# Performance work log

Measured on AMD Instinct MI355X. Metric: run time of the kernel, lower is better.

Reference implementation:

```python
import jax, jax.numpy as jnp
import numpy as np


def setup_inputs() -> dict:
    key = jax.random.key(0)
    ks = jax.random.split(key, 7)
    B, HW, C, H = 32, 3136, 512, 128
    return {
        "c_embed": jax.random.normal(ks[0], (B * HW, C), dtype=jnp.float32),
        "w_embed": jax.random.normal(ks[1], (B * HW, C), dtype=jnp.float32),
        "h_embed": jax.random.normal(ks[2], (B * HW, C), dtype=jnp.float32),
        "fc1_w": jax.random.normal(ks[3], (H, C), dtype=jnp.float32) * 0.05,
        "fc1_b": jax.random.normal(ks[4], (H,), dtype=jnp.float32) * 0.05,
        "fc2_w": jax.random.normal(ks[5], (3 * C, H), dtype=jnp.float32) * 0.05,
        "fc2_b": jax.random.normal(ks[6], (3 * C,), dtype=jnp.float32) * 0.05,
        "B": 32,
    }


def reference(c_embed, w_embed, h_embed, fc1_w, fc1_b, fc2_w, fc2_b, B):
    N, C = c_embed.shape
    HW = N // B
    # (1) global mean over HW of the sum of the three embeddings -> (B, C)
    s = (c_embed + w_embed + h_embed).reshape(B, HW, C).mean(axis=1)
    # (2) 2-layer MLP: fc1 -> GELU(tanh approx, matching gelu_fast) -> fc2
    y1 = jax.nn.gelu(s @ fc1_w.T + fc1_b, approximate=True)          # (B, hidden)
    logits = y1 @ fc2_w.T + fc2_b                                    # (B, 3*C)
    # (3) 3-way softmax: kernel indexes logits[j*C + c] => layout (B, 3, C),
    #     softmax over the 3 branches
    w = jax.nn.softmax(logits.reshape(B, 3, C), axis=1)              # (B, 3, C)
    w0 = jnp.repeat(w[:, 0, :], HW, axis=0)                          # (B*HW, C)
    w1 = jnp.repeat(w[:, 1, :], HW, axis=0)
    w2 = jnp.repeat(w[:, 2, :], HW, axis=0)
    # (4) broadcast weighted sum
    return c_embed * w0 + w_embed * w1 + h_embed * w2
```

## Files before the change

### kernel.cpp

```cpp
#include <hip/hip_runtime.h>

#define B_      32
#define HW_     3136
#define C_      512
#define H_      128
#define NCHUNK  32
#define ROWS_PER_CHUNK (HW_ / NCHUNK)

__global__ __launch_bounds__(256) void ps_kernel(
    const float* __restrict__ c_e,
    const float* __restrict__ w_e,
    const float* __restrict__ h_e,
    float* __restrict__ partial)
{
    const int blk = blockIdx.x;
    const int b   = blk / NCHUNK;
    const int k   = blk - b * NCHUNK;
    const int t   = threadIdx.x;

    const long row0 = (long)b * HW_ + (long)k * ROWS_PER_CHUNK;
    const float2* __restrict__ c2 = (const float2*)c_e;
    const float2* __restrict__ w2 = (const float2*)w_e;
    const float2* __restrict__ h2 = (const float2*)h_e;

    long base = row0 * (C_ / 2) + t;
    float ax = 0.f, ay = 0.f;
    #pragma unroll 2
    for (int r = 0; r < ROWS_PER_CHUNK; ++r) {
        float2 a = c2[base];
        float2 v = w2[base];
        float2 u = h2[base];
        ax += a.x + v.x + u.x;
        ay += a.y + v.y + u.y;
        base += (C_ / 2);
    }
    float2 o; o.x = ax; o.y = ay;
    ((float2*)partial)[(long)blk * (C_ / 2) + t] = o;
}

__global__ __launch_bounds__(256) void mlp_kernel(
    const float* __restrict__ partial,
    const float* __restrict__ fc1_w,
    const float* __restrict__ fc1_b,
    const float* __restrict__ fc2_w,
    const float* __restrict__ fc2_b,
    float* __restrict__ wbuf)
{
    __shared__ float s_lds[C_];
    __shared__ float y_lds[H_];

    const int b = blockIdx.x;
    const int t = threadIdx.x;

    for (int c = t; c < C_; c += 256) {
        float acc = 0.f;
        #pragma unroll
        for (int k = 0; k < NCHUNK; ++k)
            acc += partial[(long)(b * NCHUNK + k) * C_ + c];
        s_lds[c] = acc * (1.0f / (float)HW_);
    }
    __syncthreads();

    if (t < H_) {
        float acc = fc1_b[t];
        const float* __restrict__ wr = fc1_w + (long)t * C_;
        #pragma unroll 8
        for (int c = 0; c < C_; ++c) acc += s_lds[c] * wr[c];
        const float x  = acc;
        const float u  = 0.7978845608028654f * (x + 0.044715f * x * x * x);
        y_lds[t] = 0.5f * x * (1.0f + tanhf(u));
    }
    __syncthreads();

    for (int c = t; c < C_; c += 256) {
        float lg[3];
        #pragma unroll
        for (int j = 0; j < 3; ++j) {
            const int row = j * C_ + c;
            float acc = fc2_b[row];
            const float* __restrict__ wr = fc2_w + (long)row * H_;
            #pragma unroll 8
            for (int h = 0; h < H_; ++h) acc += y_lds[h] * wr[h];
            lg[j] = acc;
        }
        const float m  = fmaxf(lg[0], fmaxf(lg[1], lg[2]));
        const float e0 = __expf(lg[0] - m);
        const float e1 = __expf(lg[1] - m);
        const float e2 = __expf(lg[2] - m);
        const float inv = 1.0f / (e0 + e1 + e2);
        float* __restrict__ wb = wbuf + (long)b * 3 * C_;
        wb[0 * C_ + c] = e0 * inv;
        wb[1 * C_ + c] = e1 * inv;
        wb[2 * C_ + c] = e2 * inv;
    }
}

__global__ __launch_bounds__(256) void out_kernel(
    const float* __restrict__ c_e,
    const float* __restrict__ w_e,
    const float* __restrict__ h_e,
    const float* __restrict__ wbuf,
    float* __restrict__ out)
{
    const float4* __restrict__ c4 = (const float4*)c_e;
    const float4* __restrict__ w4 = (const float4*)w_e;
    const float4* __restrict__ h4 = (const float4*)h_e;
    float4* __restrict__ o4       = (float4*)out;
    const float4* __restrict__ wb4 = (const float4*)wbuf;

    const int total = B_ * HW_ * (C_ / 4);
    const int stride = gridDim.x * blockDim.x;
    for (int idx = blockIdx.x * blockDim.x + threadIdx.x; idx < total; idx += stride) {
        const int row  = idx >> 7;
        const int col4 = idx & 127;
        const int b    = row / HW_;
        const float4* __restrict__ wb = wb4 + (long)b * (3 * C_ / 4);
        const float4 w0 = wb[col4];
        const float4 w1 = wb[128 + col4];
        const float4 w2 = wb[256 + col4];
        const float4 a = c4[idx];
        const float4 v = w4[idx];
        const float4 u = h4[idx];
        float4 o;
        o.x = a.x * w0.x + v.x * w1.x + u.x * w2.x;
        o.y = a.y * w0.y + v.y * w1.y + u.y * w2.y;
        o.z = a.z * w0.z + v.z * w1.z + u.z * w2.z;
        o.w = a.w * w0.w + v.w * w1.w + u.w * w2.w;
        o4[idx] = o;
    }
}

extern "C" void kernel_launch(void* const* d_in, const int* in_sizes, int n_in,
                              void* d_out, int out_size, void* d_ws, size_t ws_size,
                              hipStream_t stream)
{
    const float* c_e   = (const float*)d_in[0];
    const float* w_e   = (const float*)d_in[1];
    const float* h_e   = (const float*)d_in[2];
    const float* fc1_w = (const float*)d_in[3];
    const float* fc1_b = (const float*)d_in[4];
    const float* fc2_w = (const float*)d_in[5];
    const float* fc2_b = (const float*)d_in[6];
    float* out = (float*)d_out;

    float* partial = (float*)d_ws;
    float* wbuf    = partial + (long)B_ * NCHUNK * C_;

    ps_kernel<<<B_ * NCHUNK, 256, 0, stream>>>(c_e, w_e, h_e, partial);
    mlp_kernel<<<B_, 256, 0, stream>>>(partial, fc1_w, fc1_b, fc2_w, fc2_b, wbuf);
    out_kernel<<<2048, 256, 0, stream>>>(c_e, w_e, h_e, wbuf, out);
}
```

Measured before the change: 328.8 us.

## Widen reduction grid, vectorize to float4, and tile output kernel per batch

The partial-sum kernel now uses float4 loads. Each block splits its rows between two half-blocks and combines them in shared memory, and the chunk count rises from 32 to 98 (falling back if workspace is small) to put more blocks in flight. The output kernel becomes a 2D grid of per-batch tiles that load the softmax weights once per thread, replacing the grid-stride loop that did an integer division per element. The MLP kernel now reads a variable chunk count, so it loses the fully unrolled partial reduction and does more partial reads.

```diff
diff --git a/kernel.cpp b/kernel.cpp
--- a/kernel.cpp
+++ b/kernel.cpp
@@ -1,41 +1,46 @@
 #include <hip/hip_runtime.h>
 
-#define B_      32
-#define HW_     3136
-#define C_      512
-#define H_      128
-#define NCHUNK  32
-#define ROWS_PER_CHUNK (HW_ / NCHUNK)
+#define B_   32
+#define HW_  3136
+#define C_   512
+#define H_   128
 
 __global__ __launch_bounds__(256) void ps_kernel(
-    const float* __restrict__ c_e,
-    const float* __restrict__ w_e,
-    const float* __restrict__ h_e,
-    float* __restrict__ partial)
+    const float4* __restrict__ c4,
+    const float4* __restrict__ w4,
+    const float4* __restrict__ h4,
+    float4* __restrict__ partial,
+    int rows)
 {
-    const int blk = blockIdx.x;
-    const int b   = blk / NCHUNK;
-    const int k   = blk - b * NCHUNK;
-    const int t   = threadIdx.x;
+    const int k    = blockIdx.x;
+    const int b    = blockIdx.y;
+    const int CH   = gridDim.x;
+    const int col4 = threadIdx.x & 127;
+    const int rl   = threadIdx.x >> 7;
 
-    const long row0 = (long)b * HW_ + (long)k * ROWS_PER_CHUNK;
-    const float2* __restrict__ c2 = (const float2*)c_e;
-    const float2* __restrict__ w2 = (const float2*)w_e;
-    const float2* __restrict__ h2 = (const float2*)h_e;
+    long base = ((long)b * HW_ + (long)k * rows + rl) * (C_ / 4) + col4;
+    float4 acc = make_float4(0.f, 0.f, 0.f, 0.f);
 
-    long base = row0 * (C_ / 2) + t;
-    float ax = 0.f, ay = 0.f;
-    #pragma unroll 2
-    for (int r = 0; r < ROWS_PER_CHUNK; ++r) {
-        float2 a = c2[base];
-        float2 v = w2[base];
-        float2 u = h2[base];
-        ax += a.x + v.x + u.x;
-        ay += a.y + v.y + u.y;
-        base += (C_ / 2);
+    #pragma unroll 4
+    for (int r = 0; r < rows; r += 2) {
+        const float4 a = c4[base];
+        const float4 v = w4[base];
+        const float4 u = h4[base];
+        acc.x += a.x + v.x + u.x;
+        acc.y += a.y + v.y + u.y;
+        acc.z += a.z + v.z + u.z;
+        acc.w += a.w + v.w + u.w;
+        base += 2 * (C_ / 4);
     }
-    float2 o; o.x = ax; o.y = ay;
-    ((float2*)partial)[(long)blk * (C_ / 2) + t] = o;
+
+    __shared__ float4 red[128];
+    if (rl == 1) red[col4] = acc;
+    __syncthreads();
+    if (rl == 0) {
+        const float4 o = red[col4];
+        acc.x += o.x; acc.y += o.y; acc.z += o.z; acc.w += o.w;
+        partial[((long)b * CH + k) * (C_ / 4) + col4] = acc;
+    }
 }
 
 __global__ __launch_bounds__(256) void mlp_kernel(
@@ -44,7 +49,8 @@
     const float* __restrict__ fc1_b,
     const float* __restrict__ fc2_w,
     const float* __restrict__ fc2_b,
-    float* __restrict__ wbuf)
+    float* __restrict__ wbuf,
+    int CH)
 {
     __shared__ float s_lds[C_];
     __shared__ float y_lds[H_];
@@ -54,9 +60,8 @@
 
     for (int c = t; c < C_; c += 256) {
         float acc = 0.f;
-        #pragma unroll
-        for (int k = 0; k < NCHUNK; ++k)
-            acc += partial[(long)(b * NCHUNK + k) * C_ + c];
+        const float* __restrict__ p = partial + (long)b * CH * C_ + c;
+        for (int k = 0; k < CH; ++k) acc += p[(long)k * C_];
         s_lds[c] = acc * (1.0f / (float)HW_);
     }
     __syncthreads();
@@ -66,8 +71,8 @@
         const float* __restrict__ wr = fc1_w + (long)t * C_;
         #pragma unroll 8
         for (int c = 0; c < C_; ++c) acc += s_lds[c] * wr[c];
-        const float x  = acc;
-        const float u  = 0.7978845608028654f * (x + 0.044715f * x * x * x);
+        const float x = acc;
+        const float u = 0.7978845608028654f * (x + 0.044715f * x * x * x);
         y_lds[t] = 0.5f * x * (1.0f + tanhf(u));
     }
     __syncthreads();
@@ -96,28 +101,25 @@
 }
 
 __global__ __launch_bounds__(256) void out_kernel(
-    const float* __restrict__ c_e,
-    const float* __restrict__ w_e,
-    const float* __restrict__ h_e,
-    const float* __restrict__ wbuf,
-    float* __restrict__ out)
+    const float4* __restrict__ c4,
+    const float4* __restrict__ w4,
+    const float4* __restrict__ h4,
+    const float4* __restrict__ wb4,
+    float4* __restrict__ o4)
 {
-    const float4* __restrict__ c4 = (const float4*)c_e;
-    const float4* __restrict__ w4 = (const float4*)w_e;
-    const float4* __restrict__ h4 = (const float4*)h_e;
-    float4* __restrict__ o4       = (float4*)out;
-    const float4* __restrict__ wb4 = (const float4*)wbuf;
+    const int blk  = blockIdx.x;
+    const int b    = blockIdx.y;
+    const int t    = threadIdx.x;
+    const int col4 = t & 127;
 
-    const int total = B_ * HW_ * (C_ / 4);
-    const int stride = gridDim.x * blockDim.x;
-    for (int idx = blockIdx.x * blockDim.x + threadIdx.x; idx < total; idx += stride) {
-        const int row  = idx >> 7;
-        const int col4 = idx & 127;
-        const int b    = row / HW_;
-        const float4* __restrict__ wb = wb4 + (long)b * (3 * C_ / 4);
-        const float4 w0 = wb[col4];
-        const float4 w1 = wb[128 + col4];
-        const float4 w2 = wb[256 + col4];
+    const float4* __restrict__ wb = wb4 + (long)b * (3 * C_ / 4);
+    const float4 w0 = wb[col4];
+    const float4 w1 = wb[128 + col4];
+    const float4 w2 = wb[256 + col4];
+
+    long idx = (long)b * (HW_ * (C_ / 4)) + (long)blk * 4096 + t;
+    #pragma unroll 4
+    for (int it = 0; it < 16; ++it) {
         const float4 a = c4[idx];
         const float4 v = w4[idx];
         const float4 u = h4[idx];
@@ -127,6 +129,7 @@
         o.z = a.z * w0.z + v.z * w1.z + u.z * w2.z;
         o.w = a.w * w0.w + v.w * w1.w + u.w * w2.w;
         o4[idx] = o;
+        idx += 256;
     }
 }
 
@@ -143,10 +146,23 @@
     const float* fc2_b = (const float*)d_in[6];
     float* out = (float*)d_out;
 
+    int CH = 98;
+    {
+        const size_t need98 = ((size_t)B_ * 98 * C_ + (size_t)B_ * 3 * C_) * 4;
+        const size_t need49 = ((size_t)B_ * 49 * C_ + (size_t)B_ * 3 * C_) * 4;
+        if (ws_size < need98) CH = 49;
+        if (ws_size < need49) CH = 32;
+    }
+    const int rows = HW_ / CH;
+
     float* partial = (float*)d_ws;
-    float* wbuf    = partial + (long)B_ * NCHUNK * C_;
+    float* wbuf    = partial + (long)B_ * CH * C_;
 
-    ps_kernel<<<B_ * NCHUNK, 256, 0, stream>>>(c_e, w_e, h_e, partial);
-    mlp_kernel<<<B_, 256, 0, stream>>>(partial, fc1_w, fc1_b, fc2_w, fc2_b, wbuf);
-    out_kernel<<<2048, 256, 0, stream>>>(c_e, w_e, h_e, wbuf, out);
+    ps_kernel<<<dim3(CH, B_), 256, 0, stream>>>(
+        (const float4*)c_e, (const float4*)w_e, (const float4*)h_e,
+        (float4*)partial, rows);
+    mlp_kernel<<<B_, 256, 0, stream>>>(partial, fc1_w, fc1_b, fc2_w, fc2_b, wbuf, CH);
+    out_kernel<<<dim3(98, B_), 256, 0, stream>>>(
+        (const float4*)c_e, (const float4*)w_e, (const float4*)h_e,
+        (const float4*)wbuf, (float4*)out);
 }
```

After: 390.0 us. +18.6%, slower.
